# Kernel optimization log

Hardware: AMD Instinct MI355X
Metric: run time of the kernel (lower is better)

The kernel has to match this reference:

```python
import jax, jax.numpy as jnp
import numpy as np

T_WIN, B, N_NODES, D_IN = 3, 1, 50000, 128
E_PER_T = 100000
HID, N_HEADS = 128, 8
D_K = HID // N_HEADS
SQRT_DK = float(np.sqrt(D_K))


def setup_inputs() -> dict:
    key = jax.random.key(0)
    ks = jax.random.split(key, 8)
    w_scale = 0.05
    return {
        "x": jax.random.normal(ks[0], (T_WIN, B, N_NODES, D_IN), jnp.float32),
        "edge_index": jax.random.randint(ks[1], (T_WIN, 2, E_PER_T), 0, N_NODES, jnp.int32),
        "Wq": jax.random.normal(ks[2], (D_IN, HID), jnp.float32) * w_scale,
        "bq": jnp.zeros((HID,), jnp.float32),
        "Wk": jax.random.normal(ks[3], (D_IN, HID), jnp.float32) * w_scale,
        "bk": jnp.zeros((HID,), jnp.float32),
        "Wv": jax.random.normal(ks[4], (D_IN, HID), jnp.float32) * w_scale,
        "bv": jnp.zeros((HID,), jnp.float32),
        "ln_scale": jnp.ones((HID,), jnp.float32),
        "ln_bias": jnp.zeros((HID,), jnp.float32),
        "W1": jax.random.normal(ks[5], (HID, 2 * HID), jnp.float32) * w_scale,
        "b1": jnp.zeros((2 * HID,), jnp.float32),
        "W2": jax.random.normal(ks[6], (2 * HID, HID), jnp.float32) * w_scale,
        "b2": jnp.zeros((HID,), jnp.float32),
    }


def _segment_softmax(a, seg, n):
    # a: [E, B, H], seg: [E] target node ids -> softmax per target node
    m = jax.ops.segment_max(a, seg, num_segments=n)           # [N, B, H]
    ex = jnp.exp(a - m[seg])
    s = jax.ops.segment_sum(ex, seg, num_segments=n)          # [N, B, H]
    return ex / (s[seg] + 1e-16)


def _ffn(h, ln_scale, ln_bias, W1, b1, W2, b2):
    # LayerNorm -> Linear -> GELU -> Linear, residual add (norm=True, skip=False, dropout=0)
    mu = jnp.mean(h, axis=-1, keepdims=True)
    var = jnp.mean((h - mu) ** 2, axis=-1, keepdims=True)
    hn = (h - mu) / jnp.sqrt(var + 1e-5) * ln_scale + ln_bias
    r = jax.nn.gelu(hn @ W1 + b1, approximate=False) @ W2 + b2
    return h + r


def reference(x, edge_index, Wq, bq, Wk, bk, Wv, bv, ln_scale, ln_bias, W1, b1, W2, b2):
    T, Bd, N, D = x.shape
    # per-node QKV once per time step (use_RTE=False): [T, B, N, HID]
    q_all = jnp.einsum("tbnd,dh->tbnh", x, Wq) + bq
    k_all = jnp.einsum("tbnd,dh->tbnh", x, Wk) + bk
    v_all = jnp.einsum("tbnd,dh->tbnh", x, Wv) + bv

    xs, cs, ss = [], [], []
    for t_tar in range(T):
        atts, msgs, segs = [], [], []
        for t_src in range(t_tar + 1):
            src = edge_index[t_src, 0]
            tar = edge_index[t_src, 1]
            # gather edge endpoints, edge axis leading: [E, B, H, D_K]
            q_e = jnp.take(q_all[t_tar], tar, axis=1).swapaxes(0, 1).reshape(-1, Bd, N_HEADS, D_K)
            k_e = jnp.take(k_all[t_src], src, axis=1).swapaxes(0, 1).reshape(-1, Bd, N_HEADS, D_K)
            v_e = jnp.take(v_all[t_src], src, axis=1).swapaxes(0, 1).reshape(-1, Bd, N_HEADS, D_K)
            atts.append(jnp.sum(q_e * k_e, axis=-1) / SQRT_DK)  # [E, B, H]
            msgs.append(v_e)
            segs.append(tar)
        att = jnp.concatenate(atts, axis=0)   # [Etot, B, H]
        msg = jnp.concatenate(msgs, axis=0)   # [Etot, B, H, D_K]
        seg = jnp.concatenate(segs, axis=0)   # [Etot]
        Et = att.shape[0]

        p_c = _segment_softmax(att, seg, N)
        p_s = _segment_softmax(-att, seg, N)
        res = (msg * p_c[..., None]).reshape(Et, Bd, HID)
        spu = (msg * p_s[..., None]).reshape(Et, Bd, HID)
        causal_hat = jax.ops.segment_sum(res, seg, num_segments=N).swapaxes(0, 1)    # [B, N, HID]
        spurious_hat = jax.ops.segment_sum(spu, seg, num_segments=N).swapaxes(0, 1)  # [B, N, HID]

        causal = _ffn(causal_hat + x[t_tar], ln_scale, ln_bias, W1, b1, W2, b2)
        spurious = _ffn(spurious_hat, ln_scale, ln_bias, W1, b1, W2, b2)
        xs.append(causal + spurious)
        cs.append(causal)
        ss.append(spurious)

    # pack (xs, cs, ss) as one array: [3, T, B, N, HID]
    return jnp.stack([jnp.stack(xs), jnp.stack(cs), jnp.stack(ss)])
```

## Files before the change

### kernel.cpp

```cpp
#include <hip/hip_runtime.h>
#include <math.h>

#define T_WIN   3
#define N_NODES 50000
#define HID     128
#define E_PER_T 100000
#define NH      8
#define DK      16
#define CAP     64


typedef unsigned short u16;
typedef __attribute__((ext_vector_type(8))) short bf16x8;
typedef __attribute__((ext_vector_type(4))) float f32x4;

__device__ __forceinline__ u16 f2bf(float v) {
    unsigned u = __float_as_uint(v);
    return (u16)((u + 0x7fffu + ((u >> 16) & 1u)) >> 16);
}
__device__ __forceinline__ float bf2f(u16 u) {
    return __uint_as_float(((unsigned)u) << 16);
}
__device__ __forceinline__ f32x4 mfma16(bf16x8 a, bf16x8 b, f32x4 c) {
    return __builtin_amdgcn_mfma_f32_16x16x32_bf16(a, b, c, 0, 0, 0);
}

__global__ __launch_bounds__(256) void wprep_kernel(
    const float* __restrict__ Wq, const float* __restrict__ Wk,
    const float* __restrict__ Wv, const float* __restrict__ W1,
    const float* __restrict__ W2,
    u16* __restrict__ WqTh, u16* __restrict__ WqTl,
    u16* __restrict__ WkTh, u16* __restrict__ WkTl,
    u16* __restrict__ WvTh, u16* __restrict__ WvTl,
    u16* __restrict__ W1T, u16* __restrict__ W2T)
{
    const int y = blockIdx.y;
    int i = blockIdx.x * 256 + threadIdx.x;
    if (y < 3) {
        if (i >= 128 * 128) return;
        const float* src = (y == 0) ? Wq : (y == 1) ? Wk : Wv;
        u16* hi = (y == 0) ? WqTh : (y == 1) ? WkTh : WvTh;
        u16* lo = (y == 0) ? WqTl : (y == 1) ? WkTl : WvTl;
        int r = i >> 7, c = i & 127;
        float v = src[i];
        u16 h = f2bf(v);
        hi[c * 128 + r] = h;
        lo[c * 128 + r] = f2bf(v - bf2f(h));
    } else if (y == 3) {
        if (i >= 128 * 256) return;
        int r = i >> 8, c = i & 255;
        W1T[c * 128 + r] = f2bf(W1[i]);
    } else {
        if (i >= 256 * 128) return;
        int r = i >> 7, c = i & 127;
        W2T[c * 256 + r] = f2bf(W2[i]);
    }
}

__global__ __launch_bounds__(256) void zero_counts_kernel(int* cursor)
{
    int i = blockIdx.x * 256 + threadIdx.x;
    if (i < T_WIN * N_NODES) cursor[i] = 0;
}

__global__ __launch_bounds__(256) void hist_kernel(
    const int* __restrict__ ei, int* counts)
{
    int i = blockIdx.x * 256 + threadIdx.x;
    if (i >= T_WIN * E_PER_T) return;
    int ts = i / E_PER_T;
    int e  = i - ts * E_PER_T;
    int tar = ei[(ts * 2 + 1) * E_PER_T + e];
    atomicAdd(&counts[ts * N_NODES + tar], 1);
}

__global__ __launch_bounds__(1024) void scan_kernel(
    const int* __restrict__ counts, int* __restrict__ offs)
{
    __shared__ int buf[1024];
    __shared__ int carry;
    const int ts = blockIdx.x;
    const int tid = threadIdx.x;
    if (tid == 0) carry = 0;
    __syncthreads();
    for (int base = 0; base < N_NODES; base += 1024) {
        int i = base + tid;
        int v = (i < N_NODES) ? counts[ts * N_NODES + i] : 0;
        buf[tid] = v;
        __syncthreads();
        for (int o = 1; o < 1024; o <<= 1) {
            int t = (tid >= o) ? buf[tid - o] : 0;
            __syncthreads();
            buf[tid] += t;
            __syncthreads();
        }
        int incl = buf[tid];
        if (i < N_NODES) offs[ts * (N_NODES + 1) + i] = carry + incl - v;
        __syncthreads();
        if (tid == 1023) carry += incl;
        __syncthreads();
    }
    if (tid == 0) offs[ts * (N_NODES + 1) + N_NODES] = carry;
}

__global__ __launch_bounds__(256) void copy_cursor_kernel(
    const int* __restrict__ offs, int* cursor)
{
    int i = blockIdx.x * 256 + threadIdx.x;
    if (i >= T_WIN * N_NODES) return;
    int ts = i / N_NODES;
    int n  = i - ts * N_NODES;
    cursor[i] = offs[ts * (N_NODES + 1) + n];
}

__global__ __launch_bounds__(256) void fill_kernel(
    const int* __restrict__ ei, int* cursor, int* __restrict__ srcbuf)
{
    int i = blockIdx.x * 256 + threadIdx.x;
    if (i >= T_WIN * E_PER_T) return;
    int ts = i / E_PER_T;
    int e  = i - ts * E_PER_T;
    int src = ei[(ts * 2) * E_PER_T + e];
    int tar = ei[(ts * 2 + 1) * E_PER_T + e];
    int pos = atomicAdd(&cursor[ts * N_NODES + tar], 1);
    srcbuf[ts * E_PER_T + pos] = src;
}

__global__ __launch_bounds__(256) void project_all_kernel(
    const float* __restrict__ x,
    const u16* __restrict__ QTh, const u16* __restrict__ QTl, const float* __restrict__ bq,
    const u16* __restrict__ KTh, const u16* __restrict__ KTl, const float* __restrict__ bk,
    const u16* __restrict__ VTh, const u16* __restrict__ VTl, const float* __restrict__ bv,
    u16* __restrict__ Qall, u16* __restrict__ Kall, u16* __restrict__ Vall)
{
    const int p  = blockIdx.y;
    const int ts = p / 3, mat = p - ts * 3;
    const u16 *WTh, *WTl; const float* b; u16* O;
    if (mat == 0)      { WTh = QTh; WTl = QTl; b = bq; O = Qall; }
    else if (mat == 1) { WTh = KTh; WTl = KTl; b = bk; O = Kall; }
    else               { WTh = VTh; WTl = VTl; b = bv; O = Vall; }
    const size_t NHID = (size_t)N_NODES * HID;
    const float* __restrict__ xs = x + (size_t)ts * NHID;
    O += (size_t)ts * NHID;

    __shared__ u16 xhS[64 * 128];
    __shared__ u16 xlS[64 * 128];
    const int tid = threadIdx.x;
    const int n0 = blockIdx.x * 64;

    {
        const int row = tid >> 2, q = tid & 3;
        const int n = n0 + row;
        const float4* xp = (const float4*)(xs + (size_t)n * 128 + q * 32);
        const int sbase = row * 128;
#pragma unroll
        for (int i = 0; i < 4; ++i) {
            float4 a = make_float4(0.f, 0.f, 0.f, 0.f), c = a;
            if (n < N_NODES) { a = xp[2 * i]; c = xp[2 * i + 1]; }
            float vv[8] = {a.x, a.y, a.z, a.w, c.x, c.y, c.z, c.w};
            uint4 uh, ul;
            unsigned* ph = (unsigned*)&uh;
            unsigned* pl = (unsigned*)&ul;
#pragma unroll
            for (int j = 0; j < 4; ++j) {
                u16 h0 = f2bf(vv[2 * j]), h1 = f2bf(vv[2 * j + 1]);
                ph[j] = (unsigned)h0 | ((unsigned)h1 << 16);
                u16 l0 = f2bf(vv[2 * j] - bf2f(h0));
                u16 l1 = f2bf(vv[2 * j + 1] - bf2f(h1));
                pl[j] = (unsigned)l0 | ((unsigned)l1 << 16);
            }
            int ch = (q * 4 + i) ^ (row & 15);
            *(uint4*)&xhS[sbase + ch * 8] = uh;
            *(uint4*)&xlS[sbase + ch * 8] = ul;
        }
    }
    __syncthreads();

    const int lane = tid & 63, w = tid >> 6;
    const int l15 = lane & 15, l4 = lane >> 4;
    f32x4 acc[4][2];
    const f32x4 z4 = {0.f, 0.f, 0.f, 0.f};
#pragma unroll
    for (int m = 0; m < 4; ++m)
#pragma unroll
        for (int n = 0; n < 2; ++n) acc[m][n] = z4;

#pragma unroll
    for (int ks = 0; ks < 4; ++ks) {
        const int ch = (ks * 4 + l4) ^ l15;
        bf16x8 ah[4], al[4];
#pragma unroll
        for (int m = 0; m < 4; ++m) {
            ah[m] = *(const bf16x8*)&xhS[(m * 16 + l15) * 128 + ch * 8];
            al[m] = *(const bf16x8*)&xlS[(m * 16 + l15) * 128 + ch * 8];
        }
        bf16x8 bh[2], bl[2];
#pragma unroll
        for (int n = 0; n < 2; ++n) {
            size_t wo = (size_t)(w * 32 + n * 16 + l15) * 128 + ks * 32 + l4 * 8;
            bh[n] = *(const bf16x8*)(WTh + wo);
            bl[n] = *(const bf16x8*)(WTl + wo);
        }
#pragma unroll
        for (int m = 0; m < 4; ++m)
#pragma unroll
            for (int n = 0; n < 2; ++n) {
                acc[m][n] = mfma16(ah[m], bh[n], acc[m][n]);
                acc[m][n] = mfma16(ah[m], bl[n], acc[m][n]);
                acc[m][n] = mfma16(al[m], bh[n], acc[m][n]);
            }
    }

#pragma unroll
    for (int n = 0; n < 2; ++n) {
        int c = w * 32 + n * 16 + l15;
        float bb = b[c];
#pragma unroll
        for (int m = 0; m < 4; ++m)
#pragma unroll
            for (int j = 0; j < 4; ++j) {
                int r = m * 16 + l4 * 4 + j;
                int ng = n0 + r;
                if (ng < N_NODES)
                    O[(size_t)ng * 128 + c] = f2bf(acc[m][n][j] + bb);
            }
    }
}

__global__ __launch_bounds__(256) void attn_fused_kernel(
    const u16* __restrict__ Qall, const u16* __restrict__ Kall,
    const u16* __restrict__ Vall,
    const int* __restrict__ offs, const int* __restrict__ srcbuf,
    float* __restrict__ hat_c_all, float* __restrict__ hat_s_all)
{
    __shared__ float logitS[4][CAP][NH];
    __shared__ int   srcS[4][CAP];
    const int t_tar = blockIdx.y;
    const int lane = threadIdx.x & 63;
    const int wave = threadIdx.x >> 6;
    const int node = blockIdx.x * 4 + wave;
    if (node >= N_NODES) return;

    const size_t NHID = (size_t)N_NODES * HID;
    float* __restrict__ hat_c = hat_c_all + (size_t)t_tar * NHID;
    float* __restrict__ hat_s = hat_s_all + (size_t)t_tar * NHID;
    const u16* __restrict__ Qt = Qall + (size_t)t_tar * NHID;
    const int h  = lane & 7;
    const int j8 = lane >> 3;

    float (*lg)[NH] = logitS[wave];
    int* sx = srcS[wave];

    uint4 q0, q1;
    {
        const uint4* qp = (const uint4*)(Qt + (size_t)node * HID + h * DK);
        q0 = qp[0]; q1 = qp[1];
    }

    float mx = -1e30f, mn = 1e30f;
    int base = 0;
    for (int ts = 0; ts <= t_tar; ++ts) {
        const int beg = offs[ts * (N_NODES + 1) + node];
        const int end = offs[ts * (N_NODES + 1) + node + 1];
        const u16* __restrict__ K = Kall + (size_t)ts * NHID;
        const int* __restrict__ sb = srcbuf + (size_t)ts * E_PER_T;
        for (int j = beg + j8; j < end; j += 8) {
            int idx = base + (j - beg);
            int src = sb[j];
            const uint4* kp = (const uint4*)(K + (size_t)src * HID + h * DK);
            uint4 k0 = kp[0], k1 = kp[1];
            float s = 0.f;
            const unsigned* pa = (const unsigned*)&q0;
            const unsigned* pb = (const unsigned*)&k0;
#pragma unroll
            for (int i = 0; i < 4; ++i)
                s += __uint_as_float(pa[i] << 16) * __uint_as_float(pb[i] << 16)
                   + __uint_as_float(pa[i] & 0xffff0000u) * __uint_as_float(pb[i] & 0xffff0000u);
            pa = (const unsigned*)&q1; pb = (const unsigned*)&k1;
#pragma unroll
            for (int i = 0; i < 4; ++i)
                s += __uint_as_float(pa[i] << 16) * __uint_as_float(pb[i] << 16)
                   + __uint_as_float(pa[i] & 0xffff0000u) * __uint_as_float(pb[i] & 0xffff0000u);
            s *= 0.25f;
            mx = fmaxf(mx, s);
            mn = fminf(mn, s);
            if (idx < CAP) { lg[idx][h] = s; if (h == 0) sx[idx] = src; }
        }
        base += end - beg;
    }
    const int dtot = base;
    if (dtot == 0) {
        size_t bidx = (size_t)node * HID + 2 * lane;
        *(float2*)(hat_c + bidx) = make_float2(0.f, 0.f);
        *(float2*)(hat_s + bidx) = make_float2(0.f, 0.f);
        return;
    }
#pragma unroll
    for (int o = 8; o < 64; o <<= 1) {
        mx = fmaxf(mx, __shfl_xor(mx, o));
        mn = fminf(mn, __shfl_xor(mn, o));
    }

    float sc = 0.f, ss = 0.f;
    {
        const int nfast = dtot < CAP ? dtot : CAP;
        for (int idx = j8; idx < nfast; idx += 8) {
            float a = lg[idx][h];
            sc += __expf(a - mx);
            ss += __expf(mn - a);
        }
        if (dtot > CAP) {
            int b2 = 0;
            for (int ts = 0; ts <= t_tar; ++ts) {
                const int beg = offs[ts * (N_NODES + 1) + node];
                const int end = offs[ts * (N_NODES + 1) + node + 1];
                const u16* K = Kall + (size_t)ts * NHID;
                const int* sb = srcbuf + (size_t)ts * E_PER_T;
                for (int j = beg + j8; j < end; j += 8) {
                    int idx = b2 + (j - beg);
                    if (idx >= CAP) {
                        int src = sb[j];
                        const uint4* kp = (const uint4*)(K + (size_t)src * HID + h * DK);
                        uint4 k0 = kp[0], k1 = kp[1];
                        float s = 0.f;
                        const unsigned* pa = (const unsigned*)&q0;
                        const unsigned* pb = (const unsigned*)&k0;
#pragma unroll
                        for (int i = 0; i < 4; ++i)
                            s += __uint_as_float(pa[i] << 16) * __uint_as_float(pb[i] << 16)
                               + __uint_as_float(pa[i] & 0xffff0000u) * __uint_as_float(pb[i] & 0xffff0000u);
                        pa = (const unsigned*)&q1; pb = (const unsigned*)&k1;
#pragma unroll
                        for (int i = 0; i < 4; ++i)
                            s += __uint_as_float(pa[i] << 16) * __uint_as_float(pb[i] << 16)
                               + __uint_as_float(pa[i] & 0xffff0000u) * __uint_as_float(pb[i] & 0xffff0000u);
                        s *= 0.25f;
                        sc += __expf(s - mx);
                        ss += __expf(mn - s);
                    }
                }
                b2 += end - beg;
            }
        }
    }
#pragma unroll
    for (int o = 8; o < 64; o <<= 1) {
        sc += __shfl_xor(sc, o);
        ss += __shfl_xor(ss, o);
    }

    const int h2 = lane >> 3;
    const float mc   = __shfl(mx, h2);
    const float mnn  = __shfl(mn, h2);
    const float isc  = 1.f / (__shfl(sc, h2) + 1e-16f);
    const float iss  = 1.f / (__shfl(ss, h2) + 1e-16f);

    float aC0 = 0.f, aC1 = 0.f, aS0 = 0.f, aS1 = 0.f;
    base = 0;
    for (int ts = 0; ts <= t_tar; ++ts) {
        const int beg = offs[ts * (N_NODES + 1) + node];
        const int end = offs[ts * (N_NODES + 1) + node + 1];
        const u16* __restrict__ V = Vall + (size_t)ts * NHID;
        const int* __restrict__ sb = srcbuf + (size_t)ts * E_PER_T;
        for (int j = beg; j < end; ++j) {
            int idx = base + (j - beg);
            float a; int src;
            if (idx < CAP) {
                a = lg[idx][h2];
                src = sx[idx];
            } else {
                src = sb[j];
                unsigned qd = *(const unsigned*)(Qt + (size_t)node * HID + 2 * lane);
                unsigned kd = *(const unsigned*)(Kall + (size_t)ts * NHID + (size_t)src * HID + 2 * lane);
                float p = __uint_as_float(qd << 16) * __uint_as_float(kd << 16)
                        + __uint_as_float(qd & 0xffff0000u) * __uint_as_float(kd & 0xffff0000u);
                p += __shfl_xor(p, 1);
                p += __shfl_xor(p, 2);
                p += __shfl_xor(p, 4);
                a = p * 0.25f;
            }
            float pc = __expf(a - mc) * isc;
            float ps = __expf(mnn - a) * iss;
            unsigned v2 = *(const unsigned*)(V + (size_t)src * HID + 2 * lane);
            float v0 = __uint_as_float(v2 << 16);
            float v1 = __uint_as_float(v2 & 0xffff0000u);
            aC0 += v0 * pc; aC1 += v1 * pc;
            aS0 += v0 * ps; aS1 += v1 * ps;
        }
        base += end - beg;
    }
    size_t bidx = (size_t)node * HID + 2 * lane;
    *(float2*)(hat_c + bidx) = make_float2(aC0, aC1);
    *(float2*)(hat_s + bidx) = make_float2(aS0, aS1);
}

__global__ __launch_bounds__(256, 5) void ffn_out_kernel(
    const float* __restrict__ hat_c_all, const float* __restrict__ hat_s_all,
    const float* __restrict__ x,
    const float* __restrict__ ln_s, const float* __restrict__ ln_b,
    const u16* __restrict__ W1T, const float* __restrict__ b1,
    const u16* __restrict__ W2T, const float* __restrict__ b2,
    float* __restrict__ out)
{
    __shared__ u16 hnS[2][32 * 128];
    __shared__ u16 chS[2][2][32 * 64];
    const int t_tar = blockIdx.y;
    const int n0 = blockIdx.x * 32;
    const int tid = threadIdx.x;
    const size_t NHID = (size_t)N_NODES * HID;
    const float* __restrict__ hat_c = hat_c_all + (size_t)t_tar * NHID;
    const float* __restrict__ hat_s = hat_s_all + (size_t)t_tar * NHID;
    const float* __restrict__ xt = x + (size_t)t_tar * NHID;
    const size_t TS = (size_t)T_WIN * N_NODES * HID;
    const size_t outbase = (size_t)t_tar * NHID;

    const int lane = tid & 63;
    const int wave = tid >> 6;
    const int br   = wave >> 1;
    const int wv   = wave & 1;
    const int l15 = lane & 15, l4 = lane >> 4;
    const f32x4 z4 = {0.f, 0.f, 0.f, 0.f};
    const float* __restrict__ hat = br ? hat_s : hat_c;

    {
        const int row = (tid & 127) >> 2, q = tid & 3;
        const int n = n0 + row;
        float v[32];
        float s = 0.f, s2 = 0.f;
        if (n < N_NODES) {
            const float4* hp = (const float4*)(hat + (size_t)n * 128 + q * 32);
            const float4* xp = (const float4*)(xt + (size_t)n * 128 + q * 32);
#pragma unroll
            for (int i = 0; i < 8; ++i) {
                float4 a = hp[i];
                if (br == 0) {
                    float4 bx = xp[i];
                    a.x += bx.x; a.y += bx.y; a.z += bx.z; a.w += bx.w;
                }
                v[4 * i] = a.x; v[4 * i + 1] = a.y;
                v[4 * i + 2] = a.z; v[4 * i + 3] = a.w;
                s  += a.x + a.y + a.z + a.w;
                s2 += a.x * a.x + a.y * a.y + a.z * a.z + a.w * a.w;
            }
        } else {
#pragma unroll
            for (int i = 0; i < 32; ++i) v[i] = 0.f;
        }
        s  += __shfl_xor(s, 1);  s  += __shfl_xor(s, 2);
        s2 += __shfl_xor(s2, 1); s2 += __shfl_xor(s2, 2);
        float mu  = s * (1.f / 128.f);
        float var = s2 * (1.f / 128.f) - mu * mu;
        float rstd = rsqrtf(var + 1e-5f);
        const int sbase = row * 128;
#pragma unroll
        for (int i = 0; i < 4; ++i) {
            uint4 uh; unsigned* ph = (unsigned*)&uh;
#pragma unroll
            for (int j = 0; j < 4; ++j) {
                int c0 = q * 32 + i * 8 + 2 * j;
                float h0 = (v[i * 8 + 2 * j]     - mu) * rstd * ln_s[c0]     + ln_b[c0];
                float h1 = (v[i * 8 + 2 * j + 1] - mu) * rstd * ln_s[c0 + 1] + ln_b[c0 + 1];
                if (n >= N_NODES) { h0 = 0.f; h1 = 0.f; }
                ph[j] = (unsigned)f2bf(h0) | ((unsigned)f2bf(h1) << 16);
            }
            int ch = (q * 4 + i) ^ (row & 15);
            *(uint4*)&hnS[br][sbase + ch * 8] = uh;
        }
    }
    __syncthreads();

    f32x4 a2[2][4];
#pragma unroll
    for (int m = 0; m < 2; ++m)
#pragma unroll
        for (int n = 0; n < 4; ++n) a2[m][n] = z4;

#pragma unroll
    for (int cc = 0; cc < 4; ++cc) {
        f32x4 a1[2][2];
#pragma unroll
        for (int m = 0; m < 2; ++m)
#pragma unroll
            for (int n = 0; n < 2; ++n) a1[m][n] = z4;
#pragma unroll
        for (int ks = 0; ks < 4; ++ks) {
            const int ch = (ks * 4 + l4) ^ l15;
            bf16x8 af[2];
#pragma unroll
            for (int m = 0; m < 2; ++m)
                af[m] = *(const bf16x8*)&hnS[br][(m * 16 + l15) * 128 + ch * 8];
#pragma unroll
            for (int n = 0; n < 2; ++n) {
                bf16x8 bfr = *(const bf16x8*)(W1T
                    + (size_t)(cc * 64 + wv * 32 + n * 16 + l15) * 128 + ks * 32 + l4 * 8);
#pragma unroll
                for (int m = 0; m < 2; ++m)
                    a1[m][n] = mfma16(af[m], bfr, a1[m][n]);
            }
        }
        u16* chw = &chS[cc & 1][br][0];
#pragma unroll
        for (int n = 0; n < 2; ++n) {
            int cl = wv * 32 + n * 16 + l15;
            float bb = b1[cc * 64 + cl];
#pragma unroll
            for (int m = 0; m < 2; ++m)
#pragma unroll
                for (int j = 0; j < 4; ++j) {
                    int r = m * 16 + l4 * 4 + j;
                    float zz = a1[m][n][j] + bb;
                    float g = 0.5f * zz * (1.f + erff(zz * 0.70710678118654752f));
                    chw[r * 64 + (((cl >> 3) ^ (r & 7)) * 8) + (cl & 7)] = f2bf(g);
                }
        }
        __syncthreads();
        const u16* chr = &chS[cc & 1][br][0];
#pragma unroll
        for (int ks2 = 0; ks2 < 2; ++ks2) {
            const int ch8 = (ks2 * 4 + l4) ^ (l15 & 7);
            bf16x8 af[2];
#pragma unroll
            for (int m = 0; m < 2; ++m)
                af[m] = *(const bf16x8*)&chr[(m * 16 + l15) * 64 + ch8 * 8];
#pragma unroll
            for (int n = 0; n < 4; ++n) {
                bf16x8 bfr = *(const bf16x8*)(W2T
                    + (size_t)(wv * 64 + n * 16 + l15) * 256 + cc * 64 + ks2 * 32 + l4 * 8);
#pragma unroll
                for (int m = 0; m < 2; ++m)
                    a2[m][n] = mfma16(af[m], bfr, a2[m][n]);
            }
        }
    }

    float* sxS = (float*)&hnS[0][0];
    if (br == 1) {
#pragma unroll
        for (int n = 0; n < 4; ++n) {
            int c = wv * 64 + n * 16 + l15;
            float bb = b2[c];
#pragma unroll
            for (int m = 0; m < 2; ++m)
#pragma unroll
                for (int j = 0; j < 4; ++j) {
                    int r = m * 16 + l4 * 4 + j;
                    int ng = n0 + r;
                    float val = a2[m][n][j] + bb;
                    if (ng < N_NODES) {
                        size_t idx = (size_t)ng * 128 + c;
                        val += hat_s[idx];
                        out[2 * TS + outbase + idx] = val;
                    }
                    sxS[r * 128 + c] = val;
                }
        }
    }
    __syncthreads();
    if (br == 0) {
#pragma unroll
        for (int n = 0; n < 4; ++n) {
            int c = wv * 64 + n * 16 + l15;
            float bb = b2[c];
#pragma unroll
            for (int m = 0; m < 2; ++m)
#pragma unroll
                for (int j = 0; j < 4; ++j) {
                    int r = m * 16 + l4 * 4 + j;
                    int ng = n0 + r;
                    if (ng < N_NODES) {
                        size_t idx = (size_t)ng * 128 + c;
                        float val = a2[m][n][j] + bb + hat_c[idx] + xt[idx];
                        float sv = sxS[r * 128 + c];
                        size_t o = outbase + idx;
                        out[o]      = val + sv;
                        out[TS + o] = val;
                    }
                }
        }
    }
}

extern "C" void kernel_launch(void* const* d_in, const int* in_sizes, int n_in,
                              void* d_out, int out_size, void* d_ws, size_t ws_size,
                              hipStream_t stream) {
    const float* x    = (const float*)d_in[0];
    const int*   ei   = (const int*)  d_in[1];
    const float* Wq   = (const float*)d_in[2];
    const float* bq   = (const float*)d_in[3];
    const float* Wk   = (const float*)d_in[4];
    const float* bk   = (const float*)d_in[5];
    const float* Wv   = (const float*)d_in[6];
    const float* bv   = (const float*)d_in[7];
    const float* ln_s = (const float*)d_in[8];
    const float* ln_b = (const float*)d_in[9];
    const float* W1   = (const float*)d_in[10];
    const float* b1   = (const float*)d_in[11];
    const float* W2   = (const float*)d_in[12];
    const float* b2   = (const float*)d_in[13];
    float* out = (float*)d_out;

    const size_t NHID = (size_t)N_NODES * HID;
    char* p = (char*)d_ws;
    auto alloc = [&p](size_t bytes) -> void* {
        void* r = (void*)p;
        p += (bytes + 255) & ~(size_t)255;
        return r;
    };
    float* hat_c = (float*)alloc(3 * NHID * 4);
    float* hat_s = (float*)alloc(3 * NHID * 4);
    int* offs    = (int*)alloc((size_t)T_WIN * (N_NODES + 1) * 4);
    int* cursor  = (int*)alloc((size_t)T_WIN * N_NODES * 4);
    int* srcbuf  = (int*)alloc((size_t)T_WIN * E_PER_T * 4);
    u16* WqTh = (u16*)alloc(128 * 128 * 2);
    u16* WqTl = (u16*)alloc(128 * 128 * 2);
    u16* WkTh = (u16*)alloc(128 * 128 * 2);
    u16* WkTl = (u16*)alloc(128 * 128 * 2);
    u16* WvTh = (u16*)alloc(128 * 128 * 2);
    u16* WvTl = (u16*)alloc(128 * 128 * 2);
    u16* W1T  = (u16*)alloc(128 * 256 * 2);
    u16* W2T  = (u16*)alloc(256 * 128 * 2);
    u16* Qall = (u16*)alloc(3 * NHID * 2);
    u16* Kall = (u16*)alloc(3 * NHID * 2);
    u16* Vall = (u16*)alloc(3 * NHID * 2);

    const int PROJ_BLOCKS = (N_NODES + 63) / 64;
    const int FFN_BLOCKS  = (N_NODES + 31) / 32;
    const int NODE_BLOCKS = (N_NODES + 3) / 4;
    const int TN_BLOCKS   = (T_WIN * N_NODES + 255) / 256;
    const int TE_BLOCKS   = (T_WIN * E_PER_T + 255) / 256;

    {
        dim3 wg(128, 5);
        wprep_kernel<<<wg, 256, 0, stream>>>(
            Wq, Wk, Wv, W1, W2,
            WqTh, WqTl, WkTh, WkTl, WvTh, WvTl, W1T, W2T);
    }

    zero_counts_kernel<<<TN_BLOCKS, 256, 0, stream>>>(cursor);
    hist_kernel<<<TE_BLOCKS, 256, 0, stream>>>(ei, cursor);
    scan_kernel<<<T_WIN, 1024, 0, stream>>>(cursor, offs);
    copy_cursor_kernel<<<TN_BLOCKS, 256, 0, stream>>>(offs, cursor);
    fill_kernel<<<TE_BLOCKS, 256, 0, stream>>>(ei, cursor, srcbuf);

    {
        dim3 pg(PROJ_BLOCKS, 9);
        project_all_kernel<<<pg, 256, 0, stream>>>(
            x, WqTh, WqTl, bq, WkTh, WkTl, bk, WvTh, WvTl, bv,
            Qall, Kall, Vall);
    }

    {
        dim3 ag(NODE_BLOCKS, T_WIN);
        attn_fused_kernel<<<ag, 256, 0, stream>>>(
            Qall, Kall, Vall, offs, srcbuf, hat_c, hat_s);
    }

    {
        dim3 fg(FFN_BLOCKS, T_WIN);
        ffn_out_kernel<<<fg, 256, 0, stream>>>(
            hat_c, hat_s, x, ln_s, ln_b, W1T, b1, W2T, b2, out);
    }
}
```

Baseline: 1.119 ms.

## Unroll cached-edge aggregation and keep residual in registers for vectorized output stores

```diff
diff --git a/kernel.cpp b/kernel.cpp
--- a/kernel.cpp
+++ b/kernel.cpp
@@ -284,7 +284,7 @@
             s *= 0.25f;
             mx = fmaxf(mx, s);
             mn = fminf(mn, s);
-            if (idx < CAP) { lg[idx][h] = s; if (h == 0) sx[idx] = src; }
+            if (idx < CAP) { lg[idx][h] = s; if (h == 0) sx[idx] = ts * N_NODES + src; }
         }
         base += end - beg;
     }
@@ -356,45 +356,89 @@
     const float iss  = 1.f / (__shfl(ss, h2) + 1e-16f);
 
     float aC0 = 0.f, aC1 = 0.f, aS0 = 0.f, aS1 = 0.f;
-    base = 0;
-    for (int ts = 0; ts <= t_tar; ++ts) {
-        const int beg = offs[ts * (N_NODES + 1) + node];
-        const int end = offs[ts * (N_NODES + 1) + node + 1];
-        const u16* __restrict__ V = Vall + (size_t)ts * NHID;
-        const int* __restrict__ sb = srcbuf + (size_t)ts * E_PER_T;
-        for (int j = beg; j < end; ++j) {
-            int idx = base + (j - beg);
-            float a; int src;
-            if (idx < CAP) {
-                a = lg[idx][h2];
-                src = sx[idx];
-            } else {
-                src = sb[j];
-                unsigned qd = *(const unsigned*)(Qt + (size_t)node * HID + 2 * lane);
-                unsigned kd = *(const unsigned*)(Kall + (size_t)ts * NHID + (size_t)src * HID + 2 * lane);
-                float p = __uint_as_float(qd << 16) * __uint_as_float(kd << 16)
-                        + __uint_as_float(qd & 0xffff0000u) * __uint_as_float(kd & 0xffff0000u);
-                p += __shfl_xor(p, 1);
-                p += __shfl_xor(p, 2);
-                p += __shfl_xor(p, 4);
-                a = p * 0.25f;
-            }
-            float pc = __expf(a - mc) * isc;
-            float ps = __expf(mnn - a) * iss;
-            unsigned v2 = *(const unsigned*)(V + (size_t)src * HID + 2 * lane);
-            float v0 = __uint_as_float(v2 << 16);
-            float v1 = __uint_as_float(v2 & 0xffff0000u);
-            aC0 += v0 * pc; aC1 += v1 * pc;
-            aS0 += v0 * ps; aS1 += v1 * ps;
-        }
-        base += end - beg;
+    if (dtot <= CAP) {
+        const int dl = 2 * lane;
+        for (int i0 = 0; i0 < dtot; i0 += 4) {
+            int i1 = i0 + 1, i2 = i0 + 2, i3 = i0 + 3;
+            int k1 = (i1 < dtot) ? i1 : i0;
+            int k2 = (i2 < dtot) ? i2 : i0;
+            int k3 = (i3 < dtot) ? i3 : i0;
+            float a0 = lg[i0][h2], a1 = lg[k1][h2];
+            float a2 = lg[k2][h2], a3 = lg[k3][h2];
+            int g0 = sx[i0], g1 = sx[k1], g2 = sx[k2], g3 = sx[k3];
+            unsigned w0 = *(const unsigned*)(Vall + (size_t)g0 * HID + dl);
+            unsigned w1 = *(const unsigned*)(Vall + (size_t)g1 * HID + dl);
+            unsigned w2 = *(const unsigned*)(Vall + (size_t)g2 * HID + dl);
+            unsigned w3 = *(const unsigned*)(Vall + (size_t)g3 * HID + dl);
+            float f1 = (i1 < dtot) ? 1.f : 0.f;
+            float f2 = (i2 < dtot) ? 1.f : 0.f;
+            float f3 = (i3 < dtot) ? 1.f : 0.f;
+            {
+                float pc = __expf(a0 - mc) * isc, ps = __expf(mnn - a0) * iss;
+                float v0 = __uint_as_float(w0 << 16);
+                float v1 = __uint_as_float(w0 & 0xffff0000u);
+                aC0 += v0 * pc; aC1 += v1 * pc; aS0 += v0 * ps; aS1 += v1 * ps;
+            }
+            {
+                float pc = __expf(a1 - mc) * isc * f1, ps = __expf(mnn - a1) * iss * f1;
+                float v0 = __uint_as_float(w1 << 16);
+                float v1 = __uint_as_float(w1 & 0xffff0000u);
+                aC0 += v0 * pc; aC1 += v1 * pc; aS0 += v0 * ps; aS1 += v1 * ps;
+            }
+            {
+                float pc = __expf(a2 - mc) * isc * f2, ps = __expf(mnn - a2) * iss * f2;
+                float v0 = __uint_as_float(w2 << 16);
+                float v1 = __uint_as_float(w2 & 0xffff0000u);
+                aC0 += v0 * pc; aC1 += v1 * pc; aS0 += v0 * ps; aS1 += v1 * ps;
+            }
+            {
+                float pc = __expf(a3 - mc) * isc * f3, ps = __expf(mnn - a3) * iss * f3;
+                float v0 = __uint_as_float(w3 << 16);
+                float v1 = __uint_as_float(w3 & 0xffff0000u);
+                aC0 += v0 * pc; aC1 += v1 * pc; aS0 += v0 * ps; aS1 += v1 * ps;
+            }
+        }
+    } else {
+        int b2 = 0;
+        for (int ts = 0; ts <= t_tar; ++ts) {
+            const int beg = offs[ts * (N_NODES + 1) + node];
+            const int end = offs[ts * (N_NODES + 1) + node + 1];
+            const int* __restrict__ sb = srcbuf + (size_t)ts * E_PER_T;
+            for (int j = beg; j < end; ++j) {
+                int idx = b2 + (j - beg);
+                float a; size_t gaddr;
+                if (idx < CAP) {
+                    a = lg[idx][h2];
+                    gaddr = (size_t)sx[idx] * HID;
+                } else {
+                    int src = sb[j];
+                    gaddr = ((size_t)ts * N_NODES + src) * HID;
+                    unsigned qd = *(const unsigned*)(Qt + (size_t)node * HID + 2 * lane);
+                    unsigned kd = *(const unsigned*)(Kall + gaddr + 2 * lane);
+                    float p = __uint_as_float(qd << 16) * __uint_as_float(kd << 16)
+                            + __uint_as_float(qd & 0xffff0000u) * __uint_as_float(kd & 0xffff0000u);
+                    p += __shfl_xor(p, 1);
+                    p += __shfl_xor(p, 2);
+                    p += __shfl_xor(p, 4);
+                    a = p * 0.25f;
+                }
+                float pc = __expf(a - mc) * isc;
+                float ps = __expf(mnn - a) * iss;
+                unsigned v2 = *(const unsigned*)(Vall + gaddr + 2 * lane);
+                float v0 = __uint_as_float(v2 << 16);
+                float v1 = __uint_as_float(v2 & 0xffff0000u);
+                aC0 += v0 * pc; aC1 += v1 * pc;
+                aS0 += v0 * ps; aS1 += v1 * ps;
+            }
+            b2 += end - beg;
+        }
     }
     size_t bidx = (size_t)node * HID + 2 * lane;
     *(float2*)(hat_c + bidx) = make_float2(aC0, aC1);
     *(float2*)(hat_s + bidx) = make_float2(aS0, aS1);
 }
 
-__global__ __launch_bounds__(256, 5) void ffn_out_kernel(
+__global__ __launch_bounds__(256, 4) void ffn_out_kernel(
     const float* __restrict__ hat_c_all, const float* __restrict__ hat_s_all,
     const float* __restrict__ x,
     const float* __restrict__ ln_s, const float* __restrict__ ln_b,
@@ -402,8 +446,11 @@
     const u16* __restrict__ W2T, const float* __restrict__ b2,
     float* __restrict__ out)
 {
-    __shared__ u16 hnS[2][32 * 128];
-    __shared__ u16 chS[2][2][32 * 64];
+    __shared__ char ldsbuf[32768];
+    u16* hnS = (u16*)ldsbuf;
+    u16* chS = (u16*)(ldsbuf + 16384);
+    float* rS = (float*)ldsbuf;
+
     const int t_tar = blockIdx.y;
     const int n0 = blockIdx.x * 32;
     const int tid = threadIdx.x;
@@ -420,20 +467,23 @@
     const int wv   = wave & 1;
     const int l15 = lane & 15, l4 = lane >> 4;
     const f32x4 z4 = {0.f, 0.f, 0.f, 0.f};
-    const float* __restrict__ hat = br ? hat_s : hat_c;
-
-    {
-        const int row = (tid & 127) >> 2, q = tid & 3;
-        const int n = n0 + row;
-        float v[32];
+
+    const int brL = tid >> 7;
+    const int rowL = (tid & 127) >> 2, qL = tid & 3;
+    const int nL = n0 + rowL;
+    const float* __restrict__ hatL = brL ? hat_s : hat_c;
+
+    float v[32];
+
+    {
         float s = 0.f, s2 = 0.f;
-        if (n < N_NODES) {
-            const float4* hp = (const float4*)(hat + (size_t)n * 128 + q * 32);
-            const float4* xp = (const float4*)(xt + (size_t)n * 128 + q * 32);
+        if (nL < N_NODES) {
+            const float4* hp = (const float4*)(hatL + (size_t)nL * 128 + qL * 32);
+            const float4* xp = (const float4*)(xt + (size_t)nL * 128 + qL * 32);
 #pragma unroll
             for (int i = 0; i < 8; ++i) {
                 float4 a = hp[i];
-                if (br == 0) {
+                if (brL == 0) {
                     float4 bx = xp[i];
                     a.x += bx.x; a.y += bx.y; a.z += bx.z; a.w += bx.w;
                 }
@@ -451,20 +501,20 @@
         float mu  = s * (1.f / 128.f);
         float var = s2 * (1.f / 128.f) - mu * mu;
         float rstd = rsqrtf(var + 1e-5f);
-        const int sbase = row * 128;
+        const int sbase = brL * 4096 + rowL * 128;
 #pragma unroll
         for (int i = 0; i < 4; ++i) {
             uint4 uh; unsigned* ph = (unsigned*)&uh;
 #pragma unroll
             for (int j = 0; j < 4; ++j) {
-                int c0 = q * 32 + i * 8 + 2 * j;
+                int c0 = qL * 32 + i * 8 + 2 * j;
                 float h0 = (v[i * 8 + 2 * j]     - mu) * rstd * ln_s[c0]     + ln_b[c0];
                 float h1 = (v[i * 8 + 2 * j + 1] - mu) * rstd * ln_s[c0 + 1] + ln_b[c0 + 1];
-                if (n >= N_NODES) { h0 = 0.f; h1 = 0.f; }
+                if (nL >= N_NODES) { h0 = 0.f; h1 = 0.f; }
                 ph[j] = (unsigned)f2bf(h0) | ((unsigned)f2bf(h1) << 16);
             }
-            int ch = (q * 4 + i) ^ (row & 15);
-            *(uint4*)&hnS[br][sbase + ch * 8] = uh;
+            int ch = (qL * 4 + i) ^ (rowL & 15);
+            *(uint4*)&hnS[sbase + ch * 8] = uh;
         }
     }
     __syncthreads();
@@ -488,7 +538,7 @@
             bf16x8 af[2];
 #pragma unroll
             for (int m = 0; m < 2; ++m)
-                af[m] = *(const bf16x8*)&hnS[br][(m * 16 + l15) * 128 + ch * 8];
+                af[m] = *(const bf16x8*)&hnS[br * 4096 + (m * 16 + l15) * 128 + ch * 8];
 #pragma unroll
             for (int n = 0; n < 2; ++n) {
                 bf16x8 bfr = *(const bf16x8*)(W1T
@@ -498,7 +548,7 @@
                     a1[m][n] = mfma16(af[m], bfr, a1[m][n]);
             }
         }
-        u16* chw = &chS[cc & 1][br][0];
+        u16* chw = chS + ((cc & 1) * 2 + br) * (32 * 64);
 #pragma unroll
         for (int n = 0; n < 2; ++n) {
             int cl = wv * 32 + n * 16 + l15;
@@ -514,7 +564,7 @@
                 }
         }
         __syncthreads();
-        const u16* chr = &chS[cc & 1][br][0];
+        const u16* chr = chS + ((cc & 1) * 2 + br) * (32 * 64);
 #pragma unroll
         for (int ks2 = 0; ks2 < 2; ++ks2) {
             const int ch8 = (ks2 * 4 + l4) ^ (l15 & 7);
@@ -532,50 +582,57 @@
             }
         }
     }
-
-    float* sxS = (float*)&hnS[0][0];
-    if (br == 1) {
-#pragma unroll
-        for (int n = 0; n < 4; ++n) {
-            int c = wv * 64 + n * 16 + l15;
-            float bb = b2[c];
-#pragma unroll
-            for (int m = 0; m < 2; ++m)
-#pragma unroll
-                for (int j = 0; j < 4; ++j) {
-                    int r = m * 16 + l4 * 4 + j;
-                    int ng = n0 + r;
-                    float val = a2[m][n][j] + bb;
-                    if (ng < N_NODES) {
-                        size_t idx = (size_t)ng * 128 + c;
-                        val += hat_s[idx];
-                        out[2 * TS + outbase + idx] = val;
-                    }
-                    sxS[r * 128 + c] = val;
-                }
-        }
-    }
     __syncthreads();
-    if (br == 0) {
-#pragma unroll
-        for (int n = 0; n < 4; ++n) {
-            int c = wv * 64 + n * 16 + l15;
-            float bb = b2[c];
-#pragma unroll
-            for (int m = 0; m < 2; ++m)
-#pragma unroll
-                for (int j = 0; j < 4; ++j) {
-                    int r = m * 16 + l4 * 4 + j;
-                    int ng = n0 + r;
-                    if (ng < N_NODES) {
-                        size_t idx = (size_t)ng * 128 + c;
-                        float val = a2[m][n][j] + bb + hat_c[idx] + xt[idx];
-                        float sv = sxS[r * 128 + c];
-                        size_t o = outbase + idx;
-                        out[o]      = val + sv;
-                        out[TS + o] = val;
-                    }
-                }
+
+#pragma unroll
+    for (int n = 0; n < 4; ++n) {
+        int c = wv * 64 + n * 16 + l15;
+        float bb = b2[c];
+#pragma unroll
+        for (int m = 0; m < 2; ++m)
+#pragma unroll
+            for (int j = 0; j < 4; ++j) {
+                int r = m * 16 + l4 * 4 + j;
+                rS[br * 4096 + r * 128 + (c ^ ((r & 7) << 2))] = a2[m][n][j] + bb;
+            }
+    }
+    __syncthreads();
+
+    const int swzL = (rowL & 7) << 2;
+    {
+#pragma unroll
+        for (int i = 0; i < 8; ++i) {
+            float4 rv = *(const float4*)&rS[brL * 4096 + rowL * 128
+                                            + ((qL * 32 + i * 4) ^ swzL)];
+            v[4 * i]     += rv.x; v[4 * i + 1] += rv.y;
+            v[4 * i + 2] += rv.z; v[4 * i + 3] += rv.w;
+        }
+    }
+    if (brL == 1) {
+        if (nL < N_NODES) {
+            float* o2 = out + 2 * TS + outbase + (size_t)nL * 128 + qL * 32;
+#pragma unroll
+            for (int i = 0; i < 8; ++i)
+                *(float4*)&o2[i * 4] = make_float4(v[4 * i], v[4 * i + 1],
+                                                   v[4 * i + 2], v[4 * i + 3]);
+        }
+#pragma unroll
+        for (int i = 0; i < 8; ++i)
+            *(float4*)&rS[4096 + rowL * 128 + ((qL * 32 + i * 4) ^ swzL)] =
+                make_float4(v[4 * i], v[4 * i + 1], v[4 * i + 2], v[4 * i + 3]);
+    }
+    __syncthreads();
+    if (brL == 0 && nL < N_NODES) {
+        float* o0 = out + outbase + (size_t)nL * 128 + qL * 32;
+        float* o1 = out + TS + outbase + (size_t)nL * 128 + qL * 32;
+#pragma unroll
+        for (int i = 0; i < 8; ++i) {
+            float4 sv = *(const float4*)&rS[4096 + rowL * 128
+                                            + ((qL * 32 + i * 4) ^ swzL)];
+            float4 cv = make_float4(v[4 * i], v[4 * i + 1], v[4 * i + 2], v[4 * i + 3]);
+            *(float4*)&o1[i * 4] = cv;
+            *(float4*)&o0[i * 4] = make_float4(cv.x + sv.x, cv.y + sv.y,
+                                               cv.z + sv.z, cv.w + sv.w);
         }
     }
 }
```

Measured after the change: 1.030 ms. 7.9% less time.
